# Kernel tuning notes

Measured on AMD Instinct MI355X. Metric: run time of the kernel, lower is better.

The kernel has to match this reference:

```python
import jax, jax.numpy as jnp
import numpy as np

N, DX, D, K, H = 4096, 128, 64, 256, 256
BETA = 0.25


def setup_inputs() -> dict:
    key = jax.random.key(0)
    ks = jax.random.split(key, 10)
    z_sample = jax.random.normal(ks[0], (N, D), jnp.float32)
    k_idx = jax.random.randint(ks[1], (N,), 0, K)
    k_sample = jax.nn.one_hot(k_idx, K, dtype=jnp.float32)  # carry is one-hot
    xt = jax.random.normal(ks[2], (N, DX), jnp.float32)
    mask = jax.random.bernoulli(ks[3], 0.5, (N,))
    transition = jax.random.uniform(ks[4], (N, K, K), jnp.float32, 0.01, 1.0)
    start_pk = jax.random.uniform(ks[5], (N, K), jnp.float32, 0.01, 1.0)
    start_pk = start_pk / start_pk.sum(-1, keepdims=True)
    W1 = jax.random.normal(ks[6], (D + DX, H), jnp.float32) / np.float32(np.sqrt(D + DX))
    b1 = jnp.zeros((H,), jnp.float32)
    W2 = jax.random.normal(ks[7], (H, H), jnp.float32) / np.float32(np.sqrt(H))
    b2 = jnp.zeros((H,), jnp.float32)
    W3 = jax.random.normal(ks[8], (H, D), jnp.float32) / np.float32(np.sqrt(H))
    b3 = jnp.zeros((D,), jnp.float32)
    C = jax.random.normal(ks[9], (K, D), jnp.float32)
    return dict(temp=jnp.float32(1.0), z_sample=z_sample, k_sample=k_sample, xt=xt,
                mask=mask, transition=transition, start_pk=start_pk,
                W1=W1, b1=b1, W2=W2, b2=b2, W3=W3, b3=b3, C=C, seed=0)


def reference(temp, z_sample, k_sample, xt, mask, transition, start_pk,
              W1, b1, W2, b2, W3, b3, C, seed):
    key = jax.random.key(seed)
    k_rng, z_rng, key = jax.random.split(key, 3)

    # replace non-finite carry entries (initial-step sentinel)
    zf = jnp.where(jnp.isfinite(z_sample), z_sample, jnp.zeros_like(z_sample))
    kf = jnp.where(jnp.isfinite(k_sample), k_sample, jnp.ones_like(k_sample))

    # SmallTanhNet encoder gt = ez([z, x])
    h = jnp.tanh(jnp.concatenate([zf, xt], axis=-1) @ W1 + b1)
    h = jnp.tanh(h @ W2 + b2)
    gt = h @ W3 + b3  # [N, D]

    # codebook pairwise Euclidean distance + argmin (VQ)
    diff = gt[:, None, :] - C[None, :, :]  # [N, K, D]
    distances = jnp.sqrt(jnp.sum(diff * diff, axis=-1))  # [N, K]
    qk_ind = jnp.argmin(distances, axis=-1)
    qk_sample = jax.nn.one_hot(qk_ind, K, dtype=gt.dtype)  # [N, K]

    # prior over discrete state from per-sample transition
    pk_gammat = jnp.einsum('nk,nkj->nj', kf, transition)
    pk_gammat = pk_gammat / pk_gammat.sum(axis=-1, keepdims=True)
    pk_gammat = jnp.where(jnp.isfinite(k_sample), pk_gammat, start_pk)

    # sample from prior categorical, select by mask
    pk_ind = jax.random.categorical(k_rng, jnp.log(pk_gammat), axis=-1)
    pk_sample = jax.nn.one_hot(pk_ind, K, dtype=gt.dtype)
    k_new = jnp.where(mask[:, None], qk_sample, pk_sample)

    # KL(Categorical(qk_sample) || Categorical(pk_gammat)); qk is one-hot so
    # sum q log q = 0 and KL = -sum q log p
    discrete_kl = -jnp.sum(qk_sample * jnp.log(pk_gammat), axis=-1)

    z_new = k_new @ C  # [N, D]

    sg = jax.lax.stop_gradient
    kl = jnp.sqrt(jnp.sum(jnp.abs(sg(gt) - z_new) ** 2, axis=-1))
    kl = kl + BETA * jnp.sqrt(jnp.sum(jnp.abs(gt - sg(z_new)) ** 2, axis=-1))

    return (z_new, kl + discrete_kl, discrete_kl, qk_sample)
```

## Files before the change

kernel.cpp:

```cpp
#include <hip/hip_runtime.h>
#include <cstdint>
#include <cmath>

#define NN   4096
#define DXX  128
#define DD   64
#define KK   256
#define HH   256
#define DIN  192
#define ROWS 16
#define NT   1024
#define GRID (NN/ROWS)

typedef __attribute__((ext_vector_type(8))) short short8;
typedef __attribute__((ext_vector_type(4))) float f32x4;
#define MFMA __builtin_amdgcn_mfma_f32_16x16x32_bf16

#define OW1 0
#define OW2 147456
#define OW3 344064
#define OCT 393216
#define OCN 442368

#define SW  264
#define SG  72
#define SSP 260
#define SSG 68

__device__ __forceinline__ unsigned short f2bf(float x){
  uint32_t u = __float_as_uint(x);
  return (unsigned short)((u + 0x7fffu + ((u>>16)&1u)) >> 16);
}
__device__ __forceinline__ float bf2f(unsigned short b){
  return __uint_as_float(((uint32_t)b)<<16);
}
__device__ __forceinline__ void split3(float x, unsigned short& h, unsigned short& m, unsigned short& l){
  h = f2bf(x); float r1 = x - bf2f(h);
  m = f2bf(r1); float r2 = r1 - bf2f(m);
  l = f2bf(r2);
}

__device__ __forceinline__ uint32_t rotl32(uint32_t v, uint32_t r){ return (v<<r)|(v>>(32u-r)); }
__device__ __forceinline__ void tf2x32(uint32_t k0, uint32_t k1,
                                       uint32_t x0, uint32_t x1,
                                       uint32_t& o0, uint32_t& o1){
  const uint32_t ks0=k0, ks1=k1, ks2 = k0 ^ k1 ^ 0x1BD11BDAu;
  x0 += ks0; x1 += ks1;
  x0+=x1; x1=rotl32(x1,13); x1^=x0;
  x0+=x1; x1=rotl32(x1,15); x1^=x0;
  x0+=x1; x1=rotl32(x1,26); x1^=x0;
  x0+=x1; x1=rotl32(x1, 6); x1^=x0;
  x0+=ks1; x1+=ks2+1u;
  x0+=x1; x1=rotl32(x1,17); x1^=x0;
  x0+=x1; x1=rotl32(x1,29); x1^=x0;
  x0+=x1; x1=rotl32(x1,16); x1^=x0;
  x0+=x1; x1=rotl32(x1,24); x1^=x0;
  x0+=ks2; x1+=ks0+2u;
  x0+=x1; x1=rotl32(x1,13); x1^=x0;
  x0+=x1; x1=rotl32(x1,15); x1^=x0;
  x0+=x1; x1=rotl32(x1,26); x1^=x0;
  x0+=x1; x1=rotl32(x1, 6); x1^=x0;
  x0+=ks0; x1+=ks1+3u;
  x0+=x1; x1=rotl32(x1,17); x1^=x0;
  x0+=x1; x1=rotl32(x1,29); x1^=x0;
  x0+=x1; x1=rotl32(x1,16); x1^=x0;
  x0+=x1; x1=rotl32(x1,24); x1^=x0;
  x0+=ks1; x1+=ks2+4u;
  x0+=x1; x1=rotl32(x1,13); x1^=x0;
  x0+=x1; x1=rotl32(x1,15); x1^=x0;
  x0+=x1; x1=rotl32(x1,26); x1^=x0;
  x0+=x1; x1=rotl32(x1, 6); x1^=x0;
  x0+=ks2; x1+=ks0+5u;
  o0=x0; o1=x1;
}
__device__ __forceinline__ float gumbel_of(uint32_t ka0, uint32_t ka1, uint32_t idx){
  uint32_t o0,o1; tf2x32(ka0,ka1,0u,idx,o0,o1);
  const uint32_t bits = o0 ^ o1;
  const float TINY = 1.17549435e-38f;
  const float f = __uint_as_float((bits>>9) | 0x3F800000u) - 1.0f;
  const float u = fmaxf(TINY, f + TINY);
  return -logf(-logf(u));
}

__global__ __launch_bounds__(256) void k_prep(const float* __restrict__ W1,
    const float* __restrict__ W2, const float* __restrict__ W3,
    const float* __restrict__ Cg, unsigned short* __restrict__ ws){
  const int tid = blockIdx.x*256 + threadIdx.x;
  const int S1=6144, S2=8192, S3=2048, S4=2048;
  if (tid >= S1+S2+S3+S4){
    int c = tid - (S1+S2+S3+S4);
    if (c < 256){
      float s=0.f;
      for (int d=0; d<64; ++d){ float v=Cg[(size_t)c*64+d]; s += v*v; }
      ((float*)(ws+OCN))[c] = s;
    }
    return;
  }
  const float* W; int N, KS, NTt; size_t base; int slot; bool ctm=false;
  if (tid < S1){ W=W1; N=256; KS=6; NTt=16; base=OW1; slot=tid; }
  else if (tid < S1+S2){ W=W2; N=256; KS=8; NTt=16; base=OW2; slot=tid-S1; }
  else if (tid < S1+S2+S3){ W=W3; N=64; KS=8; NTt=4; base=OW3; slot=tid-S1-S2; }
  else { W=Cg; N=64; KS=2; NTt=16; base=OCT; slot=tid-S1-S2-S3; ctm=true; }
  const int l  = slot & 63;
  const int ks = (slot>>6) % KS;
  const int ct = slot / (64*KS);
  const int c  = ct*16 + (l&15);
  const int k0 = ks*32 + 8*(l>>4);
  const size_t term = (size_t)NTt*KS*512;
  const size_t o = base + ((size_t)ct*KS + ks)*512 + (size_t)l*8;
  #pragma unroll
  for (int j=0;j<8;++j){
    float w = ctm ? W[(size_t)c*64 + (k0+j)] : W[(size_t)(k0+j)*N + c];
    unsigned short h,m,lo; split3(w,h,m,lo);
    ws[o + j]          = h;
    ws[o + term + j]   = m;
    ws[o + 2*term + j] = lo;
  }
}

__global__ __launch_bounds__(NT,4) void k_fused(
    const float* __restrict__ z, const float* __restrict__ ks,
    const float* __restrict__ xt, const void* __restrict__ maskp,
    const float* __restrict__ tr, const float* __restrict__ spk,
    const float* __restrict__ b1, const float* __restrict__ b2,
    const float* __restrict__ b3, const float* __restrict__ Cg,
    const int* __restrict__ seedp, const unsigned short* __restrict__ pws,
    float* __restrict__ out_z, float* __restrict__ out_kl,
    float* __restrict__ out_dkl, float* __restrict__ out_qk)
{
  const int t    = threadIdx.x;
  const int lane = t & 63;
  const int wv   = t >> 6;
  const int lr   = lane & 15;
  const int lg   = lane >> 4;
  const int n0   = blockIdx.x * ROWS;
  const int nw   = n0 + wv;

  __shared__ __align__(16) char smem[61952];
  unsigned short* Ah = (unsigned short*)smem;
  unsigned short* Am = Ah + 16*SW;
  unsigned short* Al = Am + 16*SW;
  unsigned short* Bh = (unsigned short*)(smem + 25344);
  unsigned short* Bm = Bh + 16*SW;
  unsigned short* Bl = Bm + 16*SW;
  float* sp  = (float*)(smem + 25344);
  float* sgt = (float*)(smem + 50688);
  unsigned short* Gh = (unsigned short*)(smem + 55040);
  unsigned short* Gm = Gh + 16*SG;
  unsigned short* Gl = Gm + 16*SG;
  __shared__ int sh_flag;
  const float* cnormp = (const float*)(pws + OCN);

  const float4 ksq = ((const float4*)ks)[(size_t)nw*(KK/4)+lane];
  int kv=0x7fffffff;
  if (isfinite(ksq.x)&&ksq.x>0.5f) kv=4*lane+0;
  if (isfinite(ksq.y)&&ksq.y>0.5f&&4*lane+1<kv) kv=4*lane+1;
  if (isfinite(ksq.z)&&ksq.z>0.5f&&4*lane+2<kv) kv=4*lane+2;
  if (isfinite(ksq.w)&&ksq.w>0.5f&&4*lane+3<kv) kv=4*lane+3;
  { unsigned long long bl=__ballot(kv!=0x7fffffff);
    if (bl){ int src=(int)__builtin_ctzll(bl); kv=__shfl(kv,src,64); } else kv=0; }
  const int kidx = kv;
  const float4 trq = ((const float4*)tr)[(size_t)nw*(KK*KK/4)+(size_t)kidx*(KK/4)+lane];
  const unsigned char mb = ((const unsigned char*)maskp)[nw];
  const uint32_t      mw32 = ((const uint32_t*)maskp)[nw];

  if (t==0) sh_flag = 0;
  __syncthreads();
  {
    const uint32_t* mwp = (const uint32_t*)maskp;
    uint32_t wd = mwp[t];
    if (wd!=0u && wd!=1u && wd!=0x3F800000u) atomicOr(&sh_flag,1);
  }

  for (int i=t; i<ROWS*DIN; i+=NT){
    int r=i/DIN, d=i%DIN; float v;
    if (d<DD){ v = z[(size_t)(n0+r)*DD+d]; if(!isfinite(v)) v=0.f; }
    else     { v = xt[(size_t)(n0+r)*DXX + (d-DD)]; }
    unsigned short h,m,l_; split3(v,h,m,l_);
    Ah[r*SW+d]=h; Am[r*SW+d]=m; Al[r*SW+d]=l_;
  }
  __syncthreads();
  const int flag = sh_flag;

  auto gemm_layer = [&](const unsigned short* Xh, const unsigned short* Xm, const unsigned short* Xl,
                        int KS, size_t wbase, const float* bias,
                        unsigned short* Yh, unsigned short* Ym, unsigned short* Yl){
    const int ct = wv;
    const size_t term = (size_t)16*KS*512;
    const float bb = bias[ct*16+lr];
    f32x4 a0 = {bb,bb,bb,bb}, a1 = {0.f,0.f,0.f,0.f};
    const int ar = lr*SW + lg*8;
    const unsigned short* p = &pws[wbase + ((size_t)ct*KS)*512 + (size_t)lane*8];
    short8 bh = *(const short8*)p, bm = *(const short8*)(p+term), bl = *(const short8*)(p+2*term);
    #pragma unroll 1
    for (int s=0; s<KS; ++s){
      short8 nbh, nbm, nbl;
      if (s+1<KS){
        const unsigned short* q = p + (size_t)(s+1)*512;
        nbh=*(const short8*)q; nbm=*(const short8*)(q+term); nbl=*(const short8*)(q+2*term);
      }
      short8 ah = *(const short8*)&Xh[ar + s*32];
      short8 am = *(const short8*)&Xm[ar + s*32];
      short8 al = *(const short8*)&Xl[ar + s*32];
      a0=MFMA(ah,bh,a0,0,0,0); a1=MFMA(ah,bm,a1,0,0,0);
      a0=MFMA(am,bh,a0,0,0,0); a1=MFMA(am,bm,a1,0,0,0);
      a0=MFMA(al,bh,a0,0,0,0); a1=MFMA(ah,bl,a1,0,0,0);
      bh=nbh; bm=nbm; bl=nbl;
    }
    #pragma unroll
    for (int j=0;j<4;++j){
      const int r = lg*4 + j;
      float h0 = tanhf(a0[j]+a1[j]);
      unsigned short hh,hm,hl; split3(h0,hh,hm,hl);
      Yh[r*SW + ct*16+lr]=hh; Ym[r*SW + ct*16+lr]=hm; Yl[r*SW + ct*16+lr]=hl;
    }
  };

  gemm_layer(Ah,Am,Al, 6, OW1, b1, Bh,Bm,Bl);
  __syncthreads();
  gemm_layer(Bh,Bm,Bl, 8, OW2, b2, Ah,Am,Al);
  __syncthreads();

  if (wv < 4){
    const int ct = wv;
    const size_t term = (size_t)4*8*512;
    const float bb = b3[ct*16+lr];
    f32x4 a0 = {bb,bb,bb,bb}, a1 = {0.f,0.f,0.f,0.f};
    const int ar = lr*SW + lg*8;
    const unsigned short* p = &pws[OW3 + ((size_t)ct*8)*512 + (size_t)lane*8];
    short8 bh = *(const short8*)p, bm = *(const short8*)(p+term), bl = *(const short8*)(p+2*term);
    #pragma unroll 1
    for (int s=0; s<8; ++s){
      short8 nbh, nbm, nbl;
      if (s+1<8){
        const unsigned short* q = p + (size_t)(s+1)*512;
        nbh=*(const short8*)q; nbm=*(const short8*)(q+term); nbl=*(const short8*)(q+2*term);
      }
      short8 ah = *(const short8*)&Ah[ar + s*32];
      short8 am = *(const short8*)&Am[ar + s*32];
      short8 al = *(const short8*)&Al[ar + s*32];
      a0=MFMA(ah,bh,a0,0,0,0); a1=MFMA(ah,bm,a1,0,0,0);
      a0=MFMA(am,bh,a0,0,0,0); a1=MFMA(am,bm,a1,0,0,0);
      a0=MFMA(al,bh,a0,0,0,0); a1=MFMA(ah,bl,a1,0,0,0);
      bh=nbh; bm=nbm; bl=nbl;
    }
    #pragma unroll
    for (int j=0;j<4;++j){
      const int r = lg*4 + j;
      float g = a0[j]+a1[j];
      sgt[r*SSG + ct*16+lr] = g;
      unsigned short gh,gm,gl; split3(g,gh,gm,gl);
      Gh[r*SG + ct*16+lr]=gh; Gm[r*SG + ct*16+lr]=gm; Gl[r*SG + ct*16+lr]=gl;
    }
  }

  uint32_t ka0,ka1;
  tf2x32(0u,(uint32_t)seedp[0],0u,0u,ka0,ka1);
  const bool m = flag ? (mb!=0) : (mw32!=0u);
  float g0=0,g1=0,g2=0,g3=0;
  if (!m){
    g0=gumbel_of(ka0,ka1,(uint32_t)(nw*KK+4*lane+0));
    g1=gumbel_of(ka0,ka1,(uint32_t)(nw*KK+4*lane+1));
    g2=gumbel_of(ka0,ka1,(uint32_t)(nw*KK+4*lane+2));
    g3=gumbel_of(ka0,ka1,(uint32_t)(nw*KK+4*lane+3));
  }
  __syncthreads();

  {
    const int ct = wv;
    const size_t term = (size_t)16*2*512;
    f32x4 s0={0.f,0.f,0.f,0.f}, s1=s0;
    const int ar = lr*SG + lg*8;
    #pragma unroll
    for (int s=0; s<2; ++s){
      short8 ah = *(const short8*)&Gh[ar + s*32];
      short8 am = *(const short8*)&Gm[ar + s*32];
      short8 al = *(const short8*)&Gl[ar + s*32];
      const unsigned short* p = &pws[OCT + ((size_t)ct*2 + s)*512 + (size_t)lane*8];
      short8 bh=*(const short8*)p, bm=*(const short8*)(p+term), bl=*(const short8*)(p+2*term);
      s0=MFMA(ah,bh,s0,0,0,0); s1=MFMA(ah,bm,s1,0,0,0);
      s0=MFMA(am,bh,s0,0,0,0); s1=MFMA(am,bm,s1,0,0,0);
      s0=MFMA(al,bh,s0,0,0,0); s1=MFMA(ah,bl,s1,0,0,0);
    }
    const float cn = cnormp[ct*16+lr];
    #pragma unroll
    for (int j=0;j<4;++j){
      const int r = lg*4 + j;
      sp[r*SSP + ct*16+lr] = cn - 2.f*(s0[j]+s1[j]);
    }
  }
  __syncthreads();

  {
    const int n = nw, r = wv;
    const float FMX = 3.402823466e38f;
    float4 dq = *(const float4*)&sp[r*SSP + 4*lane];
    float dv=dq.x; int di=4*lane;
    if (dq.y<dv){dv=dq.y;di=4*lane+1;}
    if (dq.z<dv){dv=dq.z;di=4*lane+2;}
    if (dq.w<dv){dv=dq.w;di=4*lane+3;}
    #pragma unroll
    for (int mm=32;mm;mm>>=1){
      float ov=__shfl_xor(dv,mm,64); int oi=__shfl_xor(di,mm,64);
      if (ov<dv||(ov==dv&&oi<di)){dv=ov;di=oi;}
    }
    const int i1=di;
    float v0=(4*lane+0==i1)?FMX:dq.x, v1=(4*lane+1==i1)?FMX:dq.y;
    float v2=(4*lane+2==i1)?FMX:dq.z, v3=(4*lane+3==i1)?FMX:dq.w;
    float ev=v0; int ei=4*lane;
    if (v1<ev){ev=v1;ei=4*lane+1;}
    if (v2<ev){ev=v2;ei=4*lane+2;}
    if (v3<ev){ev=v3;ei=4*lane+3;}
    #pragma unroll
    for (int mm=32;mm;mm>>=1){
      float ov=__shfl_xor(ev,mm,64); int oi=__shfl_xor(ei,mm,64);
      if (ov<ev||(ov==ev&&oi<ei)){ev=ov;ei=oi;}
    }
    const int i2=ei;
    const float gd = sgt[r*SSG + lane];
    float e1 = gd - Cg[(size_t)i1*DD + lane];
    float e2 = gd - Cg[(size_t)i2*DD + lane];
    float s1 = e1*e1, s2 = e2*e2;
    #pragma unroll
    for (int mm=32;mm;mm>>=1){ s1 += __shfl_xor(s1,mm,64); s2 += __shfl_xor(s2,mm,64); }
    const float D1 = sqrtf(s1), D2 = sqrtf(s2);
    const int qk = (D2<D1 || (D2==D1 && i2<i1)) ? i2 : i1;

    float s=((trq.x+trq.y)+trq.z)+trq.w;
    #pragma unroll
    for (int mm=32;mm;mm>>=1) s+=__shfl_xor(s,mm,64);
    float q0=trq.x/s, q1=trq.y/s, q2=trq.z/s, q3=trq.w/s;
    { bool f0=isfinite(ksq.x),f1=isfinite(ksq.y),f2=isfinite(ksq.z),f3=isfinite(ksq.w);
      if (__any(!(f0&&f1&&f2&&f3))){
        float4 sq=((const float4*)spk)[(size_t)n*(KK/4)+lane];
        if(!f0)q0=sq.x; if(!f1)q1=sq.y; if(!f2)q2=sq.z; if(!f3)q3=sq.w;
      } }
    const float lp0=logf(q0), lp1=logf(q1), lp2=logf(q2), lp3=logf(q3);
    const int jq=qk&3;
    float lps=(jq==0)?lp0:((jq==1)?lp1:((jq==2)?lp2:lp3));
    const float logqk=__shfl(lps,qk>>2,64);

    int sel;
    if (m){ sel=qk; }
    else {
      float sc=g0+lp0; int si=4*lane;
      { float g=g1+lp1; if(g>sc){sc=g;si=4*lane+1;} }
      { float g=g2+lp2; if(g>sc){sc=g;si=4*lane+2;} }
      { float g=g3+lp3; if(g>sc){sc=g;si=4*lane+3;} }
      #pragma unroll
      for (int mm=32;mm;mm>>=1){
        float ov=__shfl_xor(sc,mm,64); int oi=__shfl_xor(si,mm,64);
        if (ov>sc||(ov==sc&&oi<si)){sc=ov;si=oi;}
      }
      sel=si;
    }

    ((float4*)out_qk)[(size_t)n*(KK/4)+lane]=make_float4(
      (4*lane+0==qk)?1.f:0.f,(4*lane+1==qk)?1.f:0.f,
      (4*lane+2==qk)?1.f:0.f,(4*lane+3==qk)?1.f:0.f);

    const float c=Cg[(size_t)sel*DD+lane];
    out_z[(size_t)n*DD+lane]=c;
    float df = sgt[r*SSG + lane] - c;
    float p=df*df;
    #pragma unroll
    for (int mm=32;mm;mm>>=1) p+=__shfl_xor(p,mm,64);
    if (lane==0){
      float tt=sqrtf(p);
      float dkl=-logqk;
      out_kl[n]=(tt+0.25f*tt)+dkl;
      out_dkl[n]=dkl;
    }
  }
}

extern "C" void kernel_launch(void* const* d_in, const int* in_sizes, int n_in,
                              void* d_out, int out_size, void* d_ws, size_t ws_size,
                              hipStream_t stream){
  const float* z    = (const float*)d_in[1];
  const float* ksm  = (const float*)d_in[2];
  const float* xt   = (const float*)d_in[3];
  const void*  mask = d_in[4];
  const float* tr   = (const float*)d_in[5];
  const float* spk  = (const float*)d_in[6];
  const float* W1   = (const float*)d_in[7];
  const float* b1   = (const float*)d_in[8];
  const float* W2   = (const float*)d_in[9];
  const float* b2   = (const float*)d_in[10];
  const float* W3   = (const float*)d_in[11];
  const float* b3   = (const float*)d_in[12];
  const float* C    = (const float*)d_in[13];
  const int*   seed = (const int*)d_in[14];

  float* out_z   = (float*)d_out;
  float* out_kl  = out_z   + (size_t)NN*DD;
  float* out_dkl = out_kl  + NN;
  float* out_qk  = out_dkl + NN;

  unsigned short* ws = (unsigned short*)d_ws;
  k_prep<<<73,256,0,stream>>>(W1, W2, W3, C, ws);
  k_fused<<<GRID,NT,0,stream>>>(z, ksm, xt, mask, tr, spk,
                                b1, b2, b3, C, seed, ws,
                                out_z, out_kl, out_dkl, out_qk);
}
```

Baseline: 30.99 us.

## Process 32 rows per block so each weight fragment feeds two MFMA tiles

Each block now handles 32 rows instead of 16. Every wave computes two 16-row MFMA tiles against the same loaded weight fragment, which halves weight traffic from the workspace per row and halves the grid to 128 blocks. Shared memory doubles to about 121 KB, so fewer blocks fit per CU and the grid no longer covers all CUs on the chip. Separately, the weight-preparation kernel packs its three split outputs into vector short8 stores instead of scalar stores.

```diff
diff --git a/kernel.cpp b/kernel.cpp
--- a/kernel.cpp
+++ b/kernel.cpp
@@ -8,7 +8,7 @@
 #define KK   256
 #define HH   256
 #define DIN  192
-#define ROWS 16
+#define ROWS 32
 #define NT   1024
 #define GRID (NN/ROWS)
 
@@ -108,14 +108,16 @@
   const int k0 = ks*32 + 8*(l>>4);
   const size_t term = (size_t)NTt*KS*512;
   const size_t o = base + ((size_t)ct*KS + ks)*512 + (size_t)l*8;
+  short8 hv, mv, lv;
   #pragma unroll
   for (int j=0;j<8;++j){
     float w = ctm ? W[(size_t)c*64 + (k0+j)] : W[(size_t)(k0+j)*N + c];
     unsigned short h,m,lo; split3(w,h,m,lo);
-    ws[o + j]          = h;
-    ws[o + term + j]   = m;
-    ws[o + 2*term + j] = lo;
-  }
+    hv[j]=(short)h; mv[j]=(short)m; lv[j]=(short)lo;
+  }
+  *(short8*)&ws[o]          = hv;
+  *(short8*)&ws[o + term]   = mv;
+  *(short8*)&ws[o + 2*term] = lv;
 }
 
 __global__ __launch_bounds__(NT,4) void k_fused(
@@ -134,35 +136,43 @@
   const int lr   = lane & 15;
   const int lg   = lane >> 4;
   const int n0   = blockIdx.x * ROWS;
-  const int nw   = n0 + wv;
-
-  __shared__ __align__(16) char smem[61952];
+  const int nA   = n0 + wv;
+  const int nB   = n0 + 16 + wv;
+
+  __shared__ __align__(16) char smem[123904];
   unsigned short* Ah = (unsigned short*)smem;
-  unsigned short* Am = Ah + 16*SW;
-  unsigned short* Al = Am + 16*SW;
-  unsigned short* Bh = (unsigned short*)(smem + 25344);
-  unsigned short* Bm = Bh + 16*SW;
-  unsigned short* Bl = Bm + 16*SW;
-  float* sp  = (float*)(smem + 25344);
-  float* sgt = (float*)(smem + 50688);
-  unsigned short* Gh = (unsigned short*)(smem + 55040);
-  unsigned short* Gm = Gh + 16*SG;
-  unsigned short* Gl = Gm + 16*SG;
+  unsigned short* Am = Ah + 32*SW;
+  unsigned short* Al = Am + 32*SW;
+  unsigned short* Bh = (unsigned short*)(smem + 50688);
+  unsigned short* Bm = Bh + 32*SW;
+  unsigned short* Bl = Bm + 32*SW;
+  float* sp  = (float*)(smem + 50688);
+  float* sgt = (float*)(smem + 101376);
+  unsigned short* Gh = (unsigned short*)(smem + 110080);
+  unsigned short* Gm = Gh + 32*SG;
+  unsigned short* Gl = Gm + 32*SG;
   __shared__ int sh_flag;
   const float* cnormp = (const float*)(pws + OCN);
 
-  const float4 ksq = ((const float4*)ks)[(size_t)nw*(KK/4)+lane];
-  int kv=0x7fffffff;
-  if (isfinite(ksq.x)&&ksq.x>0.5f) kv=4*lane+0;
-  if (isfinite(ksq.y)&&ksq.y>0.5f&&4*lane+1<kv) kv=4*lane+1;
-  if (isfinite(ksq.z)&&ksq.z>0.5f&&4*lane+2<kv) kv=4*lane+2;
-  if (isfinite(ksq.w)&&ksq.w>0.5f&&4*lane+3<kv) kv=4*lane+3;
-  { unsigned long long bl=__ballot(kv!=0x7fffffff);
-    if (bl){ int src=(int)__builtin_ctzll(bl); kv=__shfl(kv,src,64); } else kv=0; }
-  const int kidx = kv;
-  const float4 trq = ((const float4*)tr)[(size_t)nw*(KK*KK/4)+(size_t)kidx*(KK/4)+lane];
-  const unsigned char mb = ((const unsigned char*)maskp)[nw];
-  const uint32_t      mw32 = ((const uint32_t*)maskp)[nw];
+  auto kidx_of=[&](const float4& kq)->int{
+    int kv=0x7fffffff;
+    if (isfinite(kq.x)&&kq.x>0.5f) kv=4*lane+0;
+    if (isfinite(kq.y)&&kq.y>0.5f&&4*lane+1<kv) kv=4*lane+1;
+    if (isfinite(kq.z)&&kq.z>0.5f&&4*lane+2<kv) kv=4*lane+2;
+    if (isfinite(kq.w)&&kq.w>0.5f&&4*lane+3<kv) kv=4*lane+3;
+    unsigned long long bl=__ballot(kv!=0x7fffffff);
+    if (bl){ int src=(int)__builtin_ctzll(bl); kv=__shfl(kv,src,64); } else kv=0;
+    return kv;
+  };
+  const float4 ksA = ((const float4*)ks)[(size_t)nA*(KK/4)+lane];
+  const float4 ksB = ((const float4*)ks)[(size_t)nB*(KK/4)+lane];
+  const int kA = kidx_of(ksA), kB = kidx_of(ksB);
+  const float4 trA = ((const float4*)tr)[(size_t)nA*(KK*KK/4)+(size_t)kA*(KK/4)+lane];
+  const float4 trB = ((const float4*)tr)[(size_t)nB*(KK*KK/4)+(size_t)kB*(KK/4)+lane];
+  const unsigned char mbA = ((const unsigned char*)maskp)[nA];
+  const unsigned char mbB = ((const unsigned char*)maskp)[nB];
+  const uint32_t      mwA = ((const uint32_t*)maskp)[nA];
+  const uint32_t      mwB = ((const uint32_t*)maskp)[nB];
 
   if (t==0) sh_flag = 0;
   __syncthreads();
@@ -188,8 +198,10 @@
     const int ct = wv;
     const size_t term = (size_t)16*KS*512;
     const float bb = bias[ct*16+lr];
-    f32x4 a0 = {bb,bb,bb,bb}, a1 = {0.f,0.f,0.f,0.f};
-    const int ar = lr*SW + lg*8;
+    f32x4 a0t0 = {bb,bb,bb,bb}, a1t0 = {0.f,0.f,0.f,0.f};
+    f32x4 a0t1 = {bb,bb,bb,bb}, a1t1 = {0.f,0.f,0.f,0.f};
+    const int ar0 = lr*SW + lg*8;
+    const int ar1 = (16+lr)*SW + lg*8;
     const unsigned short* p = &pws[wbase + ((size_t)ct*KS)*512 + (size_t)lane*8];
     short8 bh = *(const short8*)p, bm = *(const short8*)(p+term), bl = *(const short8*)(p+2*term);
     #pragma unroll 1
@@ -199,20 +211,29 @@
         const unsigned short* q = p + (size_t)(s+1)*512;
         nbh=*(const short8*)q; nbm=*(const short8*)(q+term); nbl=*(const short8*)(q+2*term);
       }
-      short8 ah = *(const short8*)&Xh[ar + s*32];
-      short8 am = *(const short8*)&Xm[ar + s*32];
-      short8 al = *(const short8*)&Xl[ar + s*32];
-      a0=MFMA(ah,bh,a0,0,0,0); a1=MFMA(ah,bm,a1,0,0,0);
-      a0=MFMA(am,bh,a0,0,0,0); a1=MFMA(am,bm,a1,0,0,0);
-      a0=MFMA(al,bh,a0,0,0,0); a1=MFMA(ah,bl,a1,0,0,0);
+      short8 ah0 = *(const short8*)&Xh[ar0 + s*32];
+      short8 am0 = *(const short8*)&Xm[ar0 + s*32];
+      short8 al0 = *(const short8*)&Xl[ar0 + s*32];
+      a0t0=MFMA(ah0,bh,a0t0,0,0,0); a1t0=MFMA(ah0,bm,a1t0,0,0,0);
+      a0t0=MFMA(am0,bh,a0t0,0,0,0); a1t0=MFMA(am0,bm,a1t0,0,0,0);
+      a0t0=MFMA(al0,bh,a0t0,0,0,0); a1t0=MFMA(ah0,bl,a1t0,0,0,0);
+      short8 ah1 = *(const short8*)&Xh[ar1 + s*32];
+      short8 am1 = *(const short8*)&Xm[ar1 + s*32];
+      short8 al1 = *(const short8*)&Xl[ar1 + s*32];
+      a0t1=MFMA(ah1,bh,a0t1,0,0,0); a1t1=MFMA(ah1,bm,a1t1,0,0,0);
+      a0t1=MFMA(am1,bh,a0t1,0,0,0); a1t1=MFMA(am1,bm,a1t1,0,0,0);
+      a0t1=MFMA(al1,bh,a0t1,0,0,0); a1t1=MFMA(ah1,bl,a1t1,0,0,0);
       bh=nbh; bm=nbm; bl=nbl;
     }
     #pragma unroll
     for (int j=0;j<4;++j){
       const int r = lg*4 + j;
-      float h0 = tanhf(a0[j]+a1[j]);
+      float h0 = tanhf(a0t0[j]+a1t0[j]);
       unsigned short hh,hm,hl; split3(h0,hh,hm,hl);
       Yh[r*SW + ct*16+lr]=hh; Ym[r*SW + ct*16+lr]=hm; Yl[r*SW + ct*16+lr]=hl;
+      float h1v = tanhf(a0t1[j]+a1t1[j]);
+      split3(h1v,hh,hm,hl);
+      Yh[(16+r)*SW + ct*16+lr]=hh; Ym[(16+r)*SW + ct*16+lr]=hm; Yl[(16+r)*SW + ct*16+lr]=hl;
     }
   };
 
@@ -225,8 +246,10 @@
     const int ct = wv;
     const size_t term = (size_t)4*8*512;
     const float bb = b3[ct*16+lr];
-    f32x4 a0 = {bb,bb,bb,bb}, a1 = {0.f,0.f,0.f,0.f};
-    const int ar = lr*SW + lg*8;
+    f32x4 a0t0 = {bb,bb,bb,bb}, a1t0 = {0.f,0.f,0.f,0.f};
+    f32x4 a0t1 = {bb,bb,bb,bb}, a1t1 = {0.f,0.f,0.f,0.f};
+    const int ar0 = lr*SW + lg*8;
+    const int ar1 = (16+lr)*SW + lg*8;
     const unsigned short* p = &pws[OW3 + ((size_t)ct*8)*512 + (size_t)lane*8];
     short8 bh = *(const short8*)p, bm = *(const short8*)(p+term), bl = *(const short8*)(p+2*term);
     #pragma unroll 1
@@ -236,63 +259,88 @@
         const unsigned short* q = p + (size_t)(s+1)*512;
         nbh=*(const short8*)q; nbm=*(const short8*)(q+term); nbl=*(const short8*)(q+2*term);
       }
-      short8 ah = *(const short8*)&Ah[ar + s*32];
-      short8 am = *(const short8*)&Am[ar + s*32];
-      short8 al = *(const short8*)&Al[ar + s*32];
-      a0=MFMA(ah,bh,a0,0,0,0); a1=MFMA(ah,bm,a1,0,0,0);
-      a0=MFMA(am,bh,a0,0,0,0); a1=MFMA(am,bm,a1,0,0,0);
-      a0=MFMA(al,bh,a0,0,0,0); a1=MFMA(ah,bl,a1,0,0,0);
+      short8 ah0 = *(const short8*)&Ah[ar0 + s*32];
+      short8 am0 = *(const short8*)&Am[ar0 + s*32];
+      short8 al0 = *(const short8*)&Al[ar0 + s*32];
+      a0t0=MFMA(ah0,bh,a0t0,0,0,0); a1t0=MFMA(ah0,bm,a1t0,0,0,0);
+      a0t0=MFMA(am0,bh,a0t0,0,0,0); a1t0=MFMA(am0,bm,a1t0,0,0,0);
+      a0t0=MFMA(al0,bh,a0t0,0,0,0); a1t0=MFMA(ah0,bl,a1t0,0,0,0);
+      short8 ah1 = *(const short8*)&Ah[ar1 + s*32];
+      short8 am1 = *(const short8*)&Am[ar1 + s*32];
+      short8 al1 = *(const short8*)&Al[ar1 + s*32];
+      a0t1=MFMA(ah1,bh,a0t1,0,0,0); a1t1=MFMA(ah1,bm,a1t1,0,0,0);
+      a0t1=MFMA(am1,bh,a0t1,0,0,0); a1t1=MFMA(am1,bm,a1t1,0,0,0);
+      a0t1=MFMA(al1,bh,a0t1,0,0,0); a1t1=MFMA(ah1,bl,a1t1,0,0,0);
       bh=nbh; bm=nbm; bl=nbl;
     }
     #pragma unroll
     for (int j=0;j<4;++j){
       const int r = lg*4 + j;
-      float g = a0[j]+a1[j];
+      float g = a0t0[j]+a1t0[j];
       sgt[r*SSG + ct*16+lr] = g;
       unsigned short gh,gm,gl; split3(g,gh,gm,gl);
       Gh[r*SG + ct*16+lr]=gh; Gm[r*SG + ct*16+lr]=gm; Gl[r*SG + ct*16+lr]=gl;
+      float g1v = a0t1[j]+a1t1[j];
+      sgt[(16+r)*SSG + ct*16+lr] = g1v;
+      split3(g1v,gh,gm,gl);
+      Gh[(16+r)*SG + ct*16+lr]=gh; Gm[(16+r)*SG + ct*16+lr]=gm; Gl[(16+r)*SG + ct*16+lr]=gl;
     }
   }
 
   uint32_t ka0,ka1;
   tf2x32(0u,(uint32_t)seedp[0],0u,0u,ka0,ka1);
-  const bool m = flag ? (mb!=0) : (mw32!=0u);
-  float g0=0,g1=0,g2=0,g3=0;
-  if (!m){
-    g0=gumbel_of(ka0,ka1,(uint32_t)(nw*KK+4*lane+0));
-    g1=gumbel_of(ka0,ka1,(uint32_t)(nw*KK+4*lane+1));
-    g2=gumbel_of(ka0,ka1,(uint32_t)(nw*KK+4*lane+2));
-    g3=gumbel_of(ka0,ka1,(uint32_t)(nw*KK+4*lane+3));
+  const bool mA = flag ? (mbA!=0) : (mwA!=0u);
+  const bool mB = flag ? (mbB!=0) : (mwB!=0u);
+  float gA0=0,gA1=0,gA2=0,gA3=0,gB0=0,gB1=0,gB2=0,gB3=0;
+  if (!mA){
+    gA0=gumbel_of(ka0,ka1,(uint32_t)(nA*KK+4*lane+0));
+    gA1=gumbel_of(ka0,ka1,(uint32_t)(nA*KK+4*lane+1));
+    gA2=gumbel_of(ka0,ka1,(uint32_t)(nA*KK+4*lane+2));
+    gA3=gumbel_of(ka0,ka1,(uint32_t)(nA*KK+4*lane+3));
+  }
+  if (!mB){
+    gB0=gumbel_of(ka0,ka1,(uint32_t)(nB*KK+4*lane+0));
+    gB1=gumbel_of(ka0,ka1,(uint32_t)(nB*KK+4*lane+1));
+    gB2=gumbel_of(ka0,ka1,(uint32_t)(nB*KK+4*lane+2));
+    gB3=gumbel_of(ka0,ka1,(uint32_t)(nB*KK+4*lane+3));
   }
   __syncthreads();
 
   {
     const int ct = wv;
     const size_t term = (size_t)16*2*512;
-    f32x4 s0={0.f,0.f,0.f,0.f}, s1=s0;
-    const int ar = lr*SG + lg*8;
+    f32x4 s0t0={0.f,0.f,0.f,0.f}, s1t0=s0t0, s0t1=s0t0, s1t1=s0t0;
+    const int ar0 = lr*SG + lg*8;
+    const int ar1 = (16+lr)*SG + lg*8;
     #pragma unroll
     for (int s=0; s<2; ++s){
-      short8 ah = *(const short8*)&Gh[ar + s*32];
-      short8 am = *(const short8*)&Gm[ar + s*32];
-      short8 al = *(const short8*)&Gl[ar + s*32];
       const unsigned short* p = &pws[OCT + ((size_t)ct*2 + s)*512 + (size_t)lane*8];
       short8 bh=*(const short8*)p, bm=*(const short8*)(p+term), bl=*(const short8*)(p+2*term);
-      s0=MFMA(ah,bh,s0,0,0,0); s1=MFMA(ah,bm,s1,0,0,0);
-      s0=MFMA(am,bh,s0,0,0,0); s1=MFMA(am,bm,s1,0,0,0);
-      s0=MFMA(al,bh,s0,0,0,0); s1=MFMA(ah,bl,s1,0,0,0);
+      short8 ah0 = *(const short8*)&Gh[ar0 + s*32];
+      short8 am0 = *(const short8*)&Gm[ar0 + s*32];
+      short8 al0 = *(const short8*)&Gl[ar0 + s*32];
+      s0t0=MFMA(ah0,bh,s0t0,0,0,0); s1t0=MFMA(ah0,bm,s1t0,0,0,0);
+      s0t0=MFMA(am0,bh,s0t0,0,0,0); s1t0=MFMA(am0,bm,s1t0,0,0,0);
+      s0t0=MFMA(al0,bh,s0t0,0,0,0); s1t0=MFMA(ah0,bl,s1t0,0,0,0);
+      short8 ah1 = *(const short8*)&Gh[ar1 + s*32];
+      short8 am1 = *(const short8*)&Gm[ar1 + s*32];
+      short8 al1 = *(const short8*)&Gl[ar1 + s*32];
+      s0t1=MFMA(ah1,bh,s0t1,0,0,0); s1t1=MFMA(ah1,bm,s1t1,0,0,0);
+      s0t1=MFMA(am1,bh,s0t1,0,0,0); s1t1=MFMA(am1,bm,s1t1,0,0,0);
+      s0t1=MFMA(al1,bh,s0t1,0,0,0); s1t1=MFMA(ah1,bl,s1t1,0,0,0);
     }
     const float cn = cnormp[ct*16+lr];
     #pragma unroll
     for (int j=0;j<4;++j){
       const int r = lg*4 + j;
-      sp[r*SSP + ct*16+lr] = cn - 2.f*(s0[j]+s1[j]);
-    }
-  }
-  __syncthreads();
-
-  {
-    const int n = nw, r = wv;
+      sp[r*SSP + ct*16+lr]      = cn - 2.f*(s0t0[j]+s1t0[j]);
+      sp[(16+r)*SSP + ct*16+lr] = cn - 2.f*(s0t1[j]+s1t1[j]);
+    }
+  }
+  __syncthreads();
+
+  auto process=[&](int n,int r,const float4& ksq,const float4& trq,bool m,
+                   float g0,float g1,float g2,float g3){
     const float FMX = 3.402823466e38f;
     float4 dq = *(const float4*)&sp[r*SSP + 4*lane];
     float dv=dq.x; int di=4*lane;
@@ -371,7 +419,9 @@
       out_kl[n]=(tt+0.25f*tt)+dkl;
       out_dkl[n]=dkl;
     }
-  }
+  };
+  process(nA, wv,    ksA, trA, mA, gA0,gA1,gA2,gA3);
+  process(nB, 16+wv, ksB, trB, mB, gB0,gB1,gB2,gB3);
 }
 
 extern "C" void kernel_launch(void* const* d_in, const int* in_sizes, int n_in,
```

Result: slower. 38.93 us (+25.6%).
